# Kernel tuning notes

Measured on AMD Instinct MI355X. Metric: run time of the kernel, lower is better.

## Reference

```python
import jax, jax.numpy as jnp
import numpy as np

B, LC, LQ, D = 256, 400, 50, 128
NEG = 1e12


def setup_inputs() -> dict:
    key = jax.random.key(0)
    ks = jax.random.split(key, 7)
    return {
        "x_cont": jax.random.normal(ks[0], (B, LC, D), dtype=jnp.float32),
        "x_ques": jax.random.normal(ks[1], (B, LQ, D), dtype=jnp.float32),
        "W0": jax.random.normal(ks[2], (D, 1), dtype=jnp.float32) * (1.0 / np.sqrt(D)),
        "W1": jax.random.normal(ks[3], (D, 1), dtype=jnp.float32) * (1.0 / np.sqrt(D)),
        "W2": jax.random.normal(ks[4], (1, 1, D), dtype=jnp.float32) * (1.0 / np.sqrt(D)),
        "cont_len": jax.random.randint(ks[5], (B, 1), 1, LC, dtype=jnp.int32),
        "ques_len": jax.random.randint(ks[6], (B, 1), 1, LQ, dtype=jnp.int32),
    }


def reference(x_cont, x_ques, W0, W1, W2, cont_len, ques_len):
    # Trilinear similarity S[b,c,q] = xc.W0 + xq.W1 + (xc*W2).xq
    s_c = x_cont @ W0                                   # (B, LC, 1)
    s_q = jnp.swapaxes(x_ques @ W1, 1, 2)               # (B, 1, LQ)
    s_f = jnp.einsum('bcd,bqd->bcq', x_cont * W2, x_ques)
    S = s_c + s_q + s_f                                 # (B, LC, LQ)

    # Length masks: position valid iff pos < seq_len (matches one_hot+cumsum)
    q_mask = (jnp.arange(LQ)[None, :] < ques_len).astype(S.dtype)  # (B, LQ)
    c_mask = (jnp.arange(LC)[None, :] < cont_len).astype(S.dtype)  # (B, LC)

    S_bar = jax.nn.softmax(S - (1.0 - q_mask)[:, None, :] * NEG, axis=-1)
    S_T = jnp.swapaxes(
        jax.nn.softmax(S - (1.0 - c_mask)[:, :, None] * NEG, axis=1), 1, 2)  # (B, LQ, LC)

    c2q = S_bar @ x_ques                                # (B, LC, D)
    q2c = (S_bar @ S_T) @ x_cont                        # (B, LC, D)

    result = jnp.concatenate(
        [x_cont, c2q, x_cont * c2q, x_cont * q2c], axis=-1)  # (B, LC, 4D)
    return result, S_bar, S_T
```

## Files before the change

### kernel.cpp

```cpp
#include <hip/hip_runtime.h>
#include <math.h>

#define B 256
#define LC 400
#define LQ 50
#define D 128
#define CT 64

__global__ __launch_bounds__(256, 2) void k_scores_rowsm(
    const float* __restrict__ xc_g, const float* __restrict__ xq_g,
    const float* __restrict__ W0, const float* __restrict__ W1,
    const float* __restrict__ W2, const int* __restrict__ ques_len,
    float* __restrict__ S_bar, float* __restrict__ S_Traw)
{
    __shared__ __align__(16) float xq[56 * 132];
    __shared__ __align__(16) float xc[CT * 132];
    __shared__ float w[3 * D];
    __shared__ float sq[56], sc[CT];
    __shared__ float sS[CT * 51];
    __shared__ float rowm[CT], rowi[CT];

    const int b = blockIdx.y;
    const int c0 = blockIdx.x * CT;
    const int t = threadIdx.x;
    const int nc = min(CT, LC - c0);
    const int qlen = ques_len[b];

    const float4* xq4g = (const float4*)(xq_g + (size_t)b * LQ * D);
    for (int i = t; i < 56 * 32; i += 256) {
        float4 v = (i < LQ * 32) ? xq4g[i] : make_float4(0.f, 0.f, 0.f, 0.f);
        ((float4*)xq)[(i >> 5) * 33 + (i & 31)] = v;
    }
    const float4* xc4g = (const float4*)(xc_g + (size_t)(b * LC + c0) * D);
    for (int i = t; i < nc * 32; i += 256)
        ((float4*)xc)[(i >> 5) * 33 + (i & 31)] = xc4g[i];
    if (t < D) { w[t] = W0[t]; w[D + t] = W1[t]; w[2 * D + t] = W2[t]; }
    __syncthreads();

    if (t < LQ) {
        const float4* r = (const float4*)(xq + t * 132);
        const float4* wv = (const float4*)(w + D);
        float4 a = {0.f, 0.f, 0.f, 0.f};
#pragma unroll
        for (int d = 0; d < 32; ++d) {
            float4 u = r[d], v = wv[d];
            a.x += u.x * v.x; a.y += u.y * v.y; a.z += u.z * v.z; a.w += u.w * v.w;
        }
        sq[t] = a.x + a.y + a.z + a.w;
    } else if (t >= 64 && t < 128) {
        const int c = t - 64;
        if (c < nc) {
            const float4* r = (const float4*)(xc + c * 132);
            const float4* wv = (const float4*)w;
            float4 a = {0.f, 0.f, 0.f, 0.f};
#pragma unroll
            for (int d = 0; d < 32; ++d) {
                float4 u = r[d], v = wv[d];
                a.x += u.x * v.x; a.y += u.y * v.y; a.z += u.z * v.z; a.w += u.w * v.w;
            }
            sc[c] = a.x + a.y + a.z + a.w;
        }
    }
    __syncthreads();
    for (int i = t; i < LQ * D; i += 256)
        xq[(i >> 7) * 132 + (i & 127)] *= w[2 * D + (i & 127)];
    __syncthreads();

    const int qg = t & 7;
    const int cg = (t >> 3) & 15;
    const int half = t >> 7;
    const int d0 = half * 16;

    float acc[4][7];
#pragma unroll
    for (int k = 0; k < 4; ++k)
#pragma unroll
        for (int j = 0; j < 7; ++j) acc[k][j] = 0.f;

    {
        const float4* xc4 = (const float4*)xc;
        const float4* xq4 = (const float4*)xq;
#pragma unroll 4
        for (int dd = 0; dd < 16; ++dd) {
            const int d4 = d0 + dd;
            const float4 a0 = xc4[(cg + 0)  * 33 + d4];
            const float4 a1 = xc4[(cg + 16) * 33 + d4];
            const float4 a2 = xc4[(cg + 32) * 33 + d4];
            const float4 a3 = xc4[(cg + 48) * 33 + d4];
#pragma unroll
            for (int j = 0; j < 7; ++j) {
                const float4 bq = xq4[(qg * 7 + j) * 33 + d4];
                acc[0][j] += a0.x*bq.x + a0.y*bq.y + a0.z*bq.z + a0.w*bq.w;
                acc[1][j] += a1.x*bq.x + a1.y*bq.y + a1.z*bq.z + a1.w*bq.w;
                acc[2][j] += a2.x*bq.x + a2.y*bq.y + a2.z*bq.z + a2.w*bq.w;
                acc[3][j] += a3.x*bq.x + a3.y*bq.y + a3.z*bq.z + a3.w*bq.w;
            }
        }
    }
    if (half) {
#pragma unroll
        for (int k = 0; k < 4; ++k) {
            const int c = cg + 16 * k;
            if (c < nc) {
#pragma unroll
                for (int j = 0; j < 7; ++j) {
                    const int q = qg * 7 + j;
                    if (q < LQ) sS[c * 51 + q] = acc[k][j];
                }
            }
        }
    }
    __syncthreads();
    if (!half) {
#pragma unroll
        for (int k = 0; k < 4; ++k) {
            const int c = cg + 16 * k;
            if (c < nc) {
                const float scc = sc[c];
#pragma unroll
                for (int j = 0; j < 7; ++j) {
                    const int q = qg * 7 + j;
                    if (q < LQ)
                        sS[c * 51 + q] = acc[k][j] + sS[c * 51 + q] + scc + sq[q];
                }
            }
        }
    }
    __syncthreads();

    float* redr = w;
    {
        const int r = t & 63, seg = t >> 6;
        const int qb = seg * 13;
        const int qe = min(qb + 13, qlen);
        float m = -INFINITY;
        for (int q = qb; q < qe; ++q) m = fmaxf(m, sS[r * 51 + q]);
        redr[t] = m;
    }
    __syncthreads();
    if (t < 64)
        rowm[t] = fmaxf(fmaxf(redr[t], redr[64 + t]),
                        fmaxf(redr[128 + t], redr[192 + t]));
    __syncthreads();
    {
        const int r = t & 63, seg = t >> 6;
        const int qb = seg * 13;
        const int qe = min(qb + 13, qlen);
        const float m = rowm[r];
        float s = 0.f;
        for (int q = qb; q < qe; ++q) s += __expf(sS[r * 51 + q] - m);
        redr[t] = s;
    }
    __syncthreads();
    if (t < 64)
        rowi[t] = 1.f / (redr[t] + redr[64 + t] + redr[128 + t] + redr[192 + t]);
    __syncthreads();

    float* Sb = S_bar + (size_t)(b * LC + c0) * LQ;
    for (int i = t; i < nc * LQ; i += 256) {
        const int c = i / LQ, q = i - c * LQ;
        Sb[i] = (q < qlen) ? __expf(sS[c * 51 + q] - rowm[c]) * rowi[c] : 0.f;
    }
    float* STb = S_Traw + (size_t)b * LQ * LC + c0;
    for (int i = t; i < LQ * 64; i += 256) {
        const int q = i >> 6, c = i & 63;
        if (c < nc) STb[q * LC + c] = sS[c * 51 + q];
    }
}

__global__ __launch_bounds__(512) void k_colsm_qc(
    float* __restrict__ S_T, const float* __restrict__ xc_g,
    const int* __restrict__ cont_len, float* __restrict__ T)
{
    __shared__ __align__(16) float sT[56 * 404];
    __shared__ float red[512];
    __shared__ float colmax[LQ], colinv[LQ];

    const int b = blockIdx.x;
    const int t = threadIdx.x;
    const int clen = cont_len[b];
    float* STb = S_T + (size_t)b * LQ * LC;

    const float4* STb4 = (const float4*)STb;
    float4* sTw = (float4*)sT;
    for (int i = t; i < LQ * 100; i += 512)
        sTw[(i / 100) * 101 + (i % 100)] = STb4[i];
    __syncthreads();

    const int qr = t / 10, g = t - qr * 10;
    if (t < 500) {
        const int cb = g * 40, ce = min(cb + 40, clen);
        float m = -INFINITY;
        for (int c = cb; c < ce; ++c) m = fmaxf(m, sT[qr * 404 + c]);
        red[t] = m;
    }
    __syncthreads();
    if (t < LQ) {
        float m = red[t * 10];
#pragma unroll
        for (int k = 1; k < 10; ++k) m = fmaxf(m, red[t * 10 + k]);
        colmax[t] = m;
    }
    __syncthreads();
    if (t < 500) {
        const int cb = g * 40, ce = min(cb + 40, clen);
        float s = 0.f;
        const float cm = colmax[qr];
        for (int c = cb; c < ce; ++c) s += __expf(sT[qr * 404 + c] - cm);
        red[t] = s;
    }
    __syncthreads();
    if (t < LQ) {
        float s = red[t * 10];
#pragma unroll
        for (int k = 1; k < 10; ++k) s += red[t * 10 + k];
        colinv[t] = 1.f / s;
    }
    __syncthreads();

    for (int i = t; i < LQ * LC; i += 512) {
        const int q = i / LC, c = i - q * LC;
        const float v = (c < clen) ? __expf(sT[q * 404 + c] - colmax[q]) * colinv[q] : 0.f;
        sT[q * 404 + c] = v;
        STb[i] = v;
    }
    __syncthreads();

    const int d4 = t & 31, qg = t >> 5;
    const int qb = qg * 4;
    float4 acc[4];
#pragma unroll
    for (int j = 0; j < 4; ++j) acc[j] = make_float4(0.f, 0.f, 0.f, 0.f);

    const float4* xcv = (const float4*)xc_g + (size_t)b * LC * 32 + d4;
    const float4* sT4 = (const float4*)sT;
    for (int c = 0; c < LC; c += 4) {
        const float4 x0 = xcv[(c + 0) * 32];
        const float4 x1 = xcv[(c + 1) * 32];
        const float4 x2 = xcv[(c + 2) * 32];
        const float4 x3 = xcv[(c + 3) * 32];
#pragma unroll
        for (int j = 0; j < 4; ++j) {
            const int q = min(qb + j, LQ - 1);
            const float4 wv = sT4[q * 101 + (c >> 2)];
            acc[j].x += wv.x * x0.x + wv.y * x1.x + wv.z * x2.x + wv.w * x3.x;
            acc[j].y += wv.x * x0.y + wv.y * x1.y + wv.z * x2.y + wv.w * x3.y;
            acc[j].z += wv.x * x0.z + wv.y * x1.z + wv.z * x2.z + wv.w * x3.z;
            acc[j].w += wv.x * x0.w + wv.y * x1.w + wv.z * x2.w + wv.w * x3.w;
        }
    }
    float4* Tb = (float4*)T + (size_t)b * LQ * 32 + d4;
#pragma unroll
    for (int j = 0; j < 4; ++j) {
        const int q = qb + j;
        if (q < LQ) Tb[q * 32] = acc[j];
    }
}

#define FMA4(A, s, V) { A.x += (s) * V.x; A.y += (s) * V.y; A.z += (s) * V.z; A.w += (s) * V.w; }

__global__ __launch_bounds__(256, 2) void k_out(
    const float* __restrict__ S_bar, const float* __restrict__ xq_g,
    const float* __restrict__ Tm, const float* __restrict__ xc_g,
    float* __restrict__ out)
{
    __shared__ __align__(16) float xqL[LQ * 132];
    __shared__ __align__(16) float TL[LQ * 132];
    __shared__ __align__(16) float sbT[LQ * 68];

    const int b = blockIdx.y;
    const int c0 = blockIdx.x * CT;
    const int t = threadIdx.x;
    const int nc = min(CT, LC - c0);

    const float4* xq4g = (const float4*)(xq_g + (size_t)b * LQ * D);
    const float4* T4g  = (const float4*)(Tm + (size_t)b * LQ * D);
    for (int i = t; i < LQ * 32; i += 256) {
        const int row = i >> 5, col = i & 31;
        ((float4*)xqL)[row * 33 + col] = xq4g[i];
        ((float4*)TL)[row * 33 + col]  = T4g[i];
    }
    const float* sb_g = S_bar + (size_t)(b * LC + c0) * LQ;
    for (int i = t; i < CT * LQ; i += 256) {
        const int c = i / LQ, q = i - c * LQ;
        sbT[q * 68 + c] = (c < nc) ? sb_g[i] : 0.f;
    }

    const int d4 = t & 31, cg = t >> 5;
    const int cbase = cg * 8;

    const float4* xcv = (const float4*)xc_g;
    float4 xcr[8];
#pragma unroll
    for (int i = 0; i < 8; ++i) {
        int row = b * LC + c0 + cbase + i;
        row = min(row, B * LC - 1);
        xcr[i] = xcv[(size_t)row * 32 + d4];
    }
    __syncthreads();

    float4 c2q[8], q2c[8];
#pragma unroll
    for (int i = 0; i < 8; ++i) {
        c2q[i] = make_float4(0.f, 0.f, 0.f, 0.f);
        q2c[i] = make_float4(0.f, 0.f, 0.f, 0.f);
    }
    const float4* xq4 = (const float4*)xqL;
    const float4* T4  = (const float4*)TL;
    const float4* sb4 = (const float4*)sbT;
    const int cb2 = cg * 2;
    for (int qq = 0; qq < LQ; ++qq) {
        const float4 xv = xq4[qq * 33 + d4];
        const float4 tv = T4[qq * 33 + d4];
        const float4 s0 = sb4[qq * 17 + cb2];
        const float4 s1 = sb4[qq * 17 + cb2 + 1];
        FMA4(c2q[0], s0.x, xv); FMA4(q2c[0], s0.x, tv);
        FMA4(c2q[1], s0.y, xv); FMA4(q2c[1], s0.y, tv);
        FMA4(c2q[2], s0.z, xv); FMA4(q2c[2], s0.z, tv);
        FMA4(c2q[3], s0.w, xv); FMA4(q2c[3], s0.w, tv);
        FMA4(c2q[4], s1.x, xv); FMA4(q2c[4], s1.x, tv);
        FMA4(c2q[5], s1.y, xv); FMA4(q2c[5], s1.y, tv);
        FMA4(c2q[6], s1.z, xv); FMA4(q2c[6], s1.z, tv);
        FMA4(c2q[7], s1.w, xv); FMA4(q2c[7], s1.w, tv);
    }

    float4* out4 = (float4*)out;
#pragma unroll
    for (int i = 0; i < 8; ++i) {
        const int c = cbase + i;
        if (c < nc) {
            const int row = b * LC + c0 + c;
            const float4 xc = xcr[i];
            float4* o = out4 + (size_t)row * 128 + d4;
            o[0] = xc;
            o[32] = c2q[i];
            o[64] = make_float4(xc.x * c2q[i].x, xc.y * c2q[i].y,
                                xc.z * c2q[i].z, xc.w * c2q[i].w);
            o[96] = make_float4(xc.x * q2c[i].x, xc.y * q2c[i].y,
                                xc.z * q2c[i].z, xc.w * q2c[i].w);
        }
    }
}

extern "C" void kernel_launch(void* const* d_in, const int* in_sizes, int n_in,
                              void* d_out, int out_size, void* d_ws, size_t ws_size,
                              hipStream_t stream)
{
    (void)in_sizes; (void)n_in; (void)out_size; (void)ws_size;
    const float* x_cont = (const float*)d_in[0];
    const float* x_ques = (const float*)d_in[1];
    const float* W0 = (const float*)d_in[2];
    const float* W1 = (const float*)d_in[3];
    const float* W2 = (const float*)d_in[4];
    const int* cont_len = (const int*)d_in[5];
    const int* ques_len = (const int*)d_in[6];

    float* out = (float*)d_out;
    float* out_res  = out;
    float* out_Sbar = out + (size_t)B * LC * 4 * D;
    float* out_ST   = out_Sbar + (size_t)B * LC * LQ;
    float* Tws = (float*)d_ws;

    k_scores_rowsm<<<dim3(7, B), 256, 0, stream>>>(x_cont, x_ques, W0, W1, W2,
                                                   ques_len, out_Sbar, out_ST);
    k_colsm_qc<<<B, 512, 0, stream>>>(out_ST, x_cont, cont_len, Tws);
    k_out<<<dim3(7, B), 256, 0, stream>>>(out_Sbar, x_ques, Tws, x_cont, out_res);
}
```

Baseline: 435.0 us.

## Fuse column softmax and S_T·x_cont into score kernel via last-block atomic counter

Merges the column-softmax/q2c-intermediate kernel into the score kernel. Each batch's seven tiles bump an atomic counter, and the last tile to finish computes the column softmax and T = S_T·x_cont. This removes one kernel launch and lets the tail work overlap with other batches' score blocks. In exchange, that tail work now runs on a single 256-thread block per batch, reading global S_T directly instead of through LDS. The counters live at the start of the output buffer, which k_out later overwrites, and need an extra zeroing launch.

Result: slower. 922.9 us (+112.2%).

```diff
diff --git a/kernel.cpp b/kernel.cpp
--- a/kernel.cpp
+++ b/kernel.cpp
@@ -7,18 +7,29 @@
 #define D 128
 #define CT 64
 
-__global__ __launch_bounds__(256, 2) void k_scores_rowsm(
+__global__ void k_zero(int* __restrict__ cnt)
+{
+    cnt[threadIdx.x] = 0;
+}
+
+__global__ __launch_bounds__(256, 2) void k_scores_fused(
     const float* __restrict__ xc_g, const float* __restrict__ xq_g,
     const float* __restrict__ W0, const float* __restrict__ W1,
-    const float* __restrict__ W2, const int* __restrict__ ques_len,
-    float* __restrict__ S_bar, float* __restrict__ S_Traw)
+    const float* __restrict__ W2, const int* __restrict__ cont_len,
+    const int* __restrict__ ques_len,
+    float* __restrict__ S_bar, float* __restrict__ S_Traw,
+    float* __restrict__ T, int* __restrict__ cnt)
 {
-    __shared__ __align__(16) float xq[56 * 132];
-    __shared__ __align__(16) float xc[CT * 132];
-    __shared__ float w[3 * D];
-    __shared__ float sq[56], sc[CT];
-    __shared__ float sS[CT * 51];
-    __shared__ float rowm[CT], rowi[CT];
+    __shared__ __align__(16) float smem[20104];
+    __shared__ int isLast;
+    float* xq   = smem;
+    float* xc   = smem + 7392;
+    float* sS   = smem + 15840;
+    float* w    = smem + 19104;
+    float* sq   = smem + 19488;
+    float* sc   = smem + 19544;
+    float* rowm = smem + 19608;
+    float* rowi = smem + 19672;
 
     const int b = blockIdx.y;
     const int c0 = blockIdx.x * CT;
@@ -166,94 +177,91 @@
         const int q = i >> 6, c = i & 63;
         if (c < nc) STb[q * LC + c] = sS[c * 51 + q];
     }
-}
-
-__global__ __launch_bounds__(512) void k_colsm_qc(
-    float* __restrict__ S_T, const float* __restrict__ xc_g,
-    const int* __restrict__ cont_len, float* __restrict__ T)
-{
-    __shared__ __align__(16) float sT[56 * 404];
-    __shared__ float red[512];
-    __shared__ float colmax[LQ], colinv[LQ];
-
-    const int b = blockIdx.x;
-    const int t = threadIdx.x;
+
+    __syncthreads();
+    if (t == 0) {
+        __threadfence();
+        isLast = (atomicAdd(&cnt[b], 1) == 6);
+    }
+    __syncthreads();
+    if (!isLast) return;
+    __threadfence();
+
+    float* sT     = smem;
+    float* colmax = smem + 20000;
+    float* colinv = smem + 20050;
+    float* redf   = smem;
     const int clen = cont_len[b];
-    float* STb = S_T + (size_t)b * LQ * LC;
-
-    const float4* STb4 = (const float4*)STb;
-    float4* sTw = (float4*)sT;
-    for (int i = t; i < LQ * 100; i += 512)
-        sTw[(i / 100) * 101 + (i % 100)] = STb4[i];
-    __syncthreads();
-
-    const int qr = t / 10, g = t - qr * 10;
-    if (t < 500) {
-        const int cb = g * 40, ce = min(cb + 40, clen);
+    float* STf = S_Traw + (size_t)b * LQ * LC;
+
+    if (t < 250) {
+        const int q = t % 50, g = t / 50;
+        const int cb = g * 80, ce = min(cb + 80, clen);
         float m = -INFINITY;
-        for (int c = cb; c < ce; ++c) m = fmaxf(m, sT[qr * 404 + c]);
-        red[t] = m;
+        for (int c = cb; c < ce; ++c) m = fmaxf(m, STf[q * LC + c]);
+        redf[t] = m;
     }
     __syncthreads();
     if (t < LQ) {
-        float m = red[t * 10];
-#pragma unroll
-        for (int k = 1; k < 10; ++k) m = fmaxf(m, red[t * 10 + k]);
+        float m = redf[t];
+#pragma unroll
+        for (int k = 1; k < 5; ++k) m = fmaxf(m, redf[k * 50 + t]);
         colmax[t] = m;
     }
     __syncthreads();
-    if (t < 500) {
-        const int cb = g * 40, ce = min(cb + 40, clen);
+    if (t < 250) {
+        const int q = t % 50, g = t / 50;
+        const int cb = g * 80, ce = min(cb + 80, clen);
         float s = 0.f;
-        const float cm = colmax[qr];
-        for (int c = cb; c < ce; ++c) s += __expf(sT[qr * 404 + c] - cm);
-        red[t] = s;
+        const float cm = colmax[q];
+        for (int c = cb; c < ce; ++c) s += __expf(STf[q * LC + c] - cm);
+        redf[t] = s;
     }
     __syncthreads();
     if (t < LQ) {
-        float s = red[t * 10];
-#pragma unroll
-        for (int k = 1; k < 10; ++k) s += red[t * 10 + k];
+        float s = redf[t];
+#pragma unroll
+        for (int k = 1; k < 5; ++k) s += redf[k * 50 + t];
         colinv[t] = 1.f / s;
     }
     __syncthreads();
 
-    for (int i = t; i < LQ * LC; i += 512) {
+    for (int i = t; i < LQ * LC; i += 256) {
         const int q = i / LC, c = i - q * LC;
-        const float v = (c < clen) ? __expf(sT[q * 404 + c] - colmax[q]) * colinv[q] : 0.f;
-        sT[q * 404 + c] = v;
-        STb[i] = v;
-    }
-    __syncthreads();
-
-    const int d4 = t & 31, qg = t >> 5;
-    const int qb = qg * 4;
-    float4 acc[4];
-#pragma unroll
-    for (int j = 0; j < 4; ++j) acc[j] = make_float4(0.f, 0.f, 0.f, 0.f);
-
-    const float4* xcv = (const float4*)xc_g + (size_t)b * LC * 32 + d4;
-    const float4* sT4 = (const float4*)sT;
+        const float v = (c < clen) ? __expf(STf[i] - colmax[q]) * colinv[q] : 0.f;
+        sT[q * 400 + c] = v;
+        STf[i] = v;
+    }
+    __syncthreads();
+
+    const int d4f = t & 31, qg2 = t >> 5;
+    float4 accf[7];
+#pragma unroll
+    for (int j = 0; j < 7; ++j) accf[j] = make_float4(0.f, 0.f, 0.f, 0.f);
+
+    const float4* xcv = (const float4*)xc_g + (size_t)b * LC * 32 + d4f;
     for (int c = 0; c < LC; c += 4) {
         const float4 x0 = xcv[(c + 0) * 32];
         const float4 x1 = xcv[(c + 1) * 32];
         const float4 x2 = xcv[(c + 2) * 32];
         const float4 x3 = xcv[(c + 3) * 32];
 #pragma unroll
-        for (int j = 0; j < 4; ++j) {
-            const int q = min(qb + j, LQ - 1);
-            const float4 wv = sT4[q * 101 + (c >> 2)];
-            acc[j].x += wv.x * x0.x + wv.y * x1.x + wv.z * x2.x + wv.w * x3.x;
-            acc[j].y += wv.x * x0.y + wv.y * x1.y + wv.z * x2.y + wv.w * x3.y;
-            acc[j].z += wv.x * x0.z + wv.y * x1.z + wv.z * x2.z + wv.w * x3.z;
-            acc[j].w += wv.x * x0.w + wv.y * x1.w + wv.z * x2.w + wv.w * x3.w;
-        }
-    }
-    float4* Tb = (float4*)T + (size_t)b * LQ * 32 + d4;
-#pragma unroll
-    for (int j = 0; j < 4; ++j) {
-        const int q = qb + j;
-        if (q < LQ) Tb[q * 32] = acc[j];
+        for (int j = 0; j < 7; ++j) {
+            const int q = qg2 * 7 + j;
+            if (q < LQ) {
+                const float4 wv = ((const float4*)(sT + q * 400))[c >> 2];
+                accf[j].x += wv.x * x0.x + wv.y * x1.x + wv.z * x2.x + wv.w * x3.x;
+                accf[j].y += wv.x * x0.y + wv.y * x1.y + wv.z * x2.y + wv.w * x3.y;
+                accf[j].z += wv.x * x0.z + wv.y * x1.z + wv.z * x2.z + wv.w * x3.z;
+                accf[j].w += wv.x * x0.w + wv.y * x1.w + wv.z * x2.w + wv.w * x3.w;
+            }
+        }
+    }
+    float4* Tb = (float4*)T + (size_t)b * LQ * 32 + d4f;
+#pragma unroll
+    for (int j = 0; j < 7; ++j) {
+        const int q = qg2 * 7 + j;
+        if (q < LQ) Tb[q * 32] = accf[j];
     }
 }
 
@@ -360,9 +368,11 @@
     float* out_Sbar = out + (size_t)B * LC * 4 * D;
     float* out_ST   = out_Sbar + (size_t)B * LC * LQ;
     float* Tws = (float*)d_ws;
-
-    k_scores_rowsm<<<dim3(7, B), 256, 0, stream>>>(x_cont, x_ques, W0, W1, W2,
-                                                   ques_len, out_Sbar, out_ST);
-    k_colsm_qc<<<B, 512, 0, stream>>>(out_ST, x_cont, cont_len, Tws);
+    int* cnt = (int*)out_res;
+
+    k_zero<<<1, 256, 0, stream>>>(cnt);
+    k_scores_fused<<<dim3(7, B), 256, 0, stream>>>(x_cont, x_ques, W0, W1, W2,
+                                                   cont_len, ques_len,
+                                                   out_Sbar, out_ST, Tws, cnt);
     k_out<<<dim3(7, B), 256, 0, stream>>>(out_Sbar, x_ques, Tws, x_cont, out_res);
 }
```
